# Kernel tuning notes

Hardware: AMD Instinct MI355X
Metric: run time of the kernel (lower is better)

Reference implementation:

```python
import jax, jax.numpy as jnp
import numpy as np

DIM = 4096
N_HEADS = 32
N_KV_HEADS = 8
HEAD_DIM = DIM // N_HEADS  # 128
N_REP = N_HEADS // N_KV_HEADS  # 4
BSZ_LIST = (16, 16)
START_POS_LIST = (2048, 1024)
SEQLEN = 1
CACHE_LEN = 2080
ROPE_THETA = 500000.0


def setup_inputs() -> dict:
    key = jax.random.key(0)
    ks = jax.random.split(key, 10)
    total_bsz = sum(BSZ_LIST)
    x = jax.random.normal(ks[0], (total_bsz, SEQLEN, DIM), dtype=jnp.float32)
    scale = 0.02
    wq = jax.random.normal(ks[1], (DIM, DIM), dtype=jnp.float32) * scale
    wk = jax.random.normal(ks[2], (N_KV_HEADS * HEAD_DIM, DIM), dtype=jnp.float32) * scale
    wv = jax.random.normal(ks[3], (N_KV_HEADS * HEAD_DIM, DIM), dtype=jnp.float32) * scale
    wo = jax.random.normal(ks[4], (DIM, DIM), dtype=jnp.float32) * scale
    cache_k0 = jax.random.normal(ks[5], (BSZ_LIST[0], CACHE_LEN, N_KV_HEADS, HEAD_DIM), dtype=jnp.float32)
    cache_v0 = jax.random.normal(ks[6], (BSZ_LIST[0], CACHE_LEN, N_KV_HEADS, HEAD_DIM), dtype=jnp.float32)
    cache_k1 = jax.random.normal(ks[7], (BSZ_LIST[1], CACHE_LEN, N_KV_HEADS, HEAD_DIM), dtype=jnp.float32)
    cache_v1 = jax.random.normal(ks[8], (BSZ_LIST[1], CACHE_LEN, N_KV_HEADS, HEAD_DIM), dtype=jnp.float32)
    # real RoPE tables (cos/sin of the complex freqs_cis)
    inv_freq = 1.0 / (ROPE_THETA ** (np.arange(0, HEAD_DIM, 2, dtype=np.float32) / HEAD_DIM))
    t = np.arange(CACHE_LEN, dtype=np.float32)
    ang = np.outer(t, inv_freq)  # [CACHE_LEN, HEAD_DIM/2]
    freqs_cos = jnp.asarray(np.cos(ang), dtype=jnp.float32)
    freqs_sin = jnp.asarray(np.sin(ang), dtype=jnp.float32)
    return {"x": x, "wq": wq, "wk": wk, "wv": wv, "wo": wo,
            "cache_k0": cache_k0, "cache_v0": cache_v0,
            "cache_k1": cache_k1, "cache_v1": cache_v1,
            "freqs_cos": freqs_cos, "freqs_sin": freqs_sin}


def _rope(v, cos, sin):
    # v: [b, s, h, d]; cos/sin: [s, d/2] -> interleaved complex rotation
    vr = v.reshape(v.shape[:-1] + (HEAD_DIM // 2, 2))
    a, b = vr[..., 0], vr[..., 1]
    c = cos[None, :, None, :]
    s = sin[None, :, None, :]
    out = jnp.stack([a * c - b * s, a * s + b * c], axis=-1)
    return out.reshape(v.shape)


def _group_attention(xq, xk, xv, cache_k, cache_v, start_pos, freqs_cos, freqs_sin):
    bsz, seqlen = xq.shape[0], xq.shape[1]
    cos = freqs_cos[start_pos:start_pos + seqlen]
    sin = freqs_sin[start_pos:start_pos + seqlen]
    xq = _rope(xq, cos, sin)
    xk = _rope(xk, cos, sin)
    # functional equivalent of cache[:, start_pos:start_pos+seqlen] = new; read [:start_pos+seqlen]
    keys = jnp.concatenate([cache_k[:, :start_pos], xk], axis=1)    # [b, kv, kvh, d]
    values = jnp.concatenate([cache_v[:, :start_pos], xv], axis=1)
    keys = jnp.repeat(keys, N_REP, axis=2)      # GQA repeat -> [b, kv, h, d]
    values = jnp.repeat(values, N_REP, axis=2)
    scores = jnp.einsum('bqhd,bkhd->bhqk', xq, keys) / jnp.sqrt(jnp.float32(HEAD_DIM))
    if seqlen > 1:
        kv_len = start_pos + seqlen
        q_pos = jnp.arange(seqlen)[:, None] + start_pos
        k_pos = jnp.arange(kv_len)[None, :]
        scores = jnp.where(k_pos <= q_pos, scores, jnp.float32(-jnp.inf))
    probs = jax.nn.softmax(scores.astype(jnp.float32), axis=-1).astype(xq.dtype)
    out = jnp.einsum('bhqk,bkhd->bqhd', probs, values)
    return out.reshape(bsz, seqlen, -1)


def reference(x, wq, wk, wv, wo, cache_k0, cache_v0, cache_k1, cache_v1, freqs_cos, freqs_sin):
    total_bsz, seqlen, _ = x.shape
    xq_ = x @ wq.T
    xk_ = x @ wk.T
    xv_ = x @ wv.T
    caches = ((cache_k0, cache_v0), (cache_k1, cache_v1))
    outputs = []
    start = 0
    for i, bsz in enumerate(BSZ_LIST):
        xq = xq_[start:start + bsz].reshape(bsz, seqlen, N_HEADS, HEAD_DIM)
        xk = xk_[start:start + bsz].reshape(bsz, seqlen, N_KV_HEADS, HEAD_DIM)
        xv = xv_[start:start + bsz].reshape(bsz, seqlen, N_KV_HEADS, HEAD_DIM)
        start += bsz
        ck, cv = caches[i]
        outputs.append(_group_attention(xq, xk, xv, ck, cv, START_POS_LIST[i], freqs_cos, freqs_sin))
    output = jnp.concatenate(outputs, axis=0)  # [total_bsz, seqlen, dim]
    return output @ wo.T
```

## Files before the change

kernel.cpp:

```cpp
#include <hip/hip_runtime.h>
#include <hip/hip_bf16.h>

#define DIM       4096
#define NHEADS    32
#define NKV       8
#define HD        128
#define NREP      4
#define CACHELEN  2080
#define QKVN      6144
#define BSZ       32
#define SP0       2048
#define SP1       1024
#define KCHUNK    256
#define SPLITROWS 128
#define MAXSPL    16
#define PSTRIDE   132

typedef unsigned short u16;
typedef unsigned int   u32;
typedef __bf16 bf16x8 __attribute__((ext_vector_type(8)));
typedef float  f32x4  __attribute__((ext_vector_type(4)));

#define LD8(dst, p) do { \
    *(float4*)(dst)       = *(const float4*)(p); \
    *(float4*)((dst) + 4) = *(const float4*)((p) + 4); } while (0)

static __device__ __forceinline__ bf16x8 pack8(float4 lo, float4 hi) {
    bf16x8 r;
    r[0] = (__bf16)lo.x; r[1] = (__bf16)lo.y; r[2] = (__bf16)lo.z; r[3] = (__bf16)lo.w;
    r[4] = (__bf16)hi.x; r[5] = (__bf16)hi.y; r[6] = (__bf16)hi.z; r[7] = (__bf16)hi.w;
    return r;
}

__global__ __launch_bounds__(256) void qkv_gemm(
    const float* __restrict__ x, const float* __restrict__ wq,
    const float* __restrict__ wk, const float* __restrict__ wv,
    float* __restrict__ qkv_acc)
{
    const int lane = threadIdx.x & 63;
    const int w    = threadIdx.x >> 6;
    const int n0   = (blockIdx.x * 4 + w) * 16;
    const float* W; int nr;
    if (n0 < 4096)      { W = wq; nr = n0; }
    else if (n0 < 5120) { W = wk; nr = n0 - 4096; }
    else                { W = wv; nr = n0 - 5120; }
    const int c16  = lane & 15;
    const int quad = lane >> 4;
    const int k0   = blockIdx.y * KCHUNK;
    const float* ap0 = x + (size_t)c16 * DIM + k0 + quad * 8;
    const float* ap1 = ap0 + 16 * DIM;
    const float* bp  = W + (size_t)(nr + c16) * DIM + k0 + quad * 8;
    f32x4 acc0 = {0.f,0.f,0.f,0.f}, acc1 = {0.f,0.f,0.f,0.f};
#pragma unroll 4
    for (int kk = 0; kk < KCHUNK; kk += 32) {
        bf16x8 a0 = pack8(*(const float4*)(ap0 + kk), *(const float4*)(ap0 + kk + 4));
        bf16x8 a1 = pack8(*(const float4*)(ap1 + kk), *(const float4*)(ap1 + kk + 4));
        bf16x8 b  = pack8(*(const float4*)(bp  + kk), *(const float4*)(bp  + kk + 4));
        acc0 = __builtin_amdgcn_mfma_f32_16x16x32_bf16(a0, b, acc0, 0, 0, 0);
        acc1 = __builtin_amdgcn_mfma_f32_16x16x32_bf16(a1, b, acc1, 0, 0, 0);
    }
#pragma unroll
    for (int r = 0; r < 4; ++r) {
        int m = quad * 4 + r;
        atomicAdd(&qkv_acc[(size_t)m * QKVN + n0 + c16], acc0[r]);
        atomicAdd(&qkv_acc[(size_t)(m + 16) * QKVN + n0 + c16], acc1[r]);
    }
}

__global__ __launch_bounds__(256) void attn_decode_split(
    const float* __restrict__ qkv,
    const float* __restrict__ ck0, const float* __restrict__ cv0,
    const float* __restrict__ ck1, const float* __restrict__ cv1,
    const float* __restrict__ fcos, const float* __restrict__ fsin,
    float* __restrict__ part)
{
    const int tid  = threadIdx.x;
    const int lane = tid & 63;
    const int w    = tid >> 6;
    const int quad = lane >> 4;
    const int ch   = lane & 15;
    const int db   = ch * 8;

    int b, g, s, sp;
    const float *CK, *CV;
    if ((int)blockIdx.x < 2048) {
        int bid = blockIdx.x;
        b = bid >> 7; g = (bid >> 4) & 7; s = bid & 15; sp = SP0;
        size_t off = (size_t)b * CACHELEN * NKV * HD;
        CK = ck0 + off; CV = cv0 + off;
    } else {
        int bid = blockIdx.x - 2048;
        b = 16 + (bid >> 6); g = (bid >> 3) & 7; s = bid & 7; sp = SP1;
        size_t off = (size_t)(b - 16) * CACHELEN * NKV * HD;
        CK = ck1 + off; CV = cv1 + off;
    }

    float cs[4], sn[4];
#pragma unroll
    for (int i = 0; i < 4; ++i) {
        int fi = sp * (HD / 2) + ch * 4 + i;
        cs[i] = fcos[fi];
        sn[i] = fsin[fi];
    }
    const float rs = 0.08838834764831845f;

    float qv[4][8];
#pragma unroll
    for (int h = 0; h < 4; ++h) {
        const float* qp = qkv + (size_t)b * QKVN + (g * 4 + h) * HD + db;
        float t[8];
#pragma unroll
        for (int j = 0; j < 8; ++j) t[j] = qp[j];
#pragma unroll
        for (int i = 0; i < 4; ++i) {
            float e = t[2 * i], o = t[2 * i + 1];
            qv[h][2 * i]     = (e * cs[i] - o * sn[i]) * rs;
            qv[h][2 * i + 1] = (e * sn[i] + o * cs[i]) * rs;
        }
    }

    float m_[4] = {-INFINITY, -INFINITY, -INFINITY, -INFINITY};
    float l_[4] = {0.f, 0.f, 0.f, 0.f};
    float acc[4][8];
#pragma unroll
    for (int h = 0; h < 4; ++h)
#pragma unroll
        for (int j = 0; j < 8; ++j) acc[h][j] = 0.f;

    const size_t rstride = NKV * HD;
    const float* kbase = CK + g * HD + db;
    const float* vbase = CV + g * HD + db;

    auto process2 = [&](const float* k0, const float* v0,
                        const float* k1, const float* v1) {
        float d[8];
#pragma unroll
        for (int i = 0; i < 8; ++i) d[i] = 0.f;
#pragma unroll
        for (int j = 0; j < 8; ++j) {
#pragma unroll
            for (int h = 0; h < 4; ++h) {
                d[h]     = fmaf(qv[h][j], k0[j], d[h]);
                d[4 + h] = fmaf(qv[h][j], k1[j], d[4 + h]);
            }
        }
#pragma unroll
        for (int off = 1; off < 16; off <<= 1) {
#pragma unroll
            for (int i = 0; i < 8; ++i) d[i] += __shfl_xor(d[i], off);
        }
#pragma unroll
        for (int h = 0; h < 4; ++h) {
            float mn = fmaxf(fmaxf(m_[h], d[h]), d[4 + h]);
            float sl = __expf(m_[h] - mn);
            float p0 = __expf(d[h] - mn);
            float p1 = __expf(d[4 + h] - mn);
            l_[h] = l_[h] * sl + p0 + p1;
#pragma unroll
            for (int j = 0; j < 8; ++j)
                acc[h][j] = fmaf(p1, v1[j], fmaf(p0, v0[j], acc[h][j] * sl));
            m_[h] = mn;
        }
    };

    {
        const int r0 = s * SPLITROWS + w * 8 + quad;
        const float* kp = kbase + (size_t)r0 * rstride;
        const float* vp = vbase + (size_t)r0 * rstride;
        float K0[8], V0[8], K1[8], V1[8];
        float nK0[8], nV0[8], nK1[8], nV1[8];
        LD8(K0, kp);
        LD8(K1, kp + 4 * rstride);
        LD8(V0, vp);
        LD8(V1, vp + 4 * rstride);
#pragma unroll
        for (int it = 0; it < 4; ++it) {
            if (it < 3) {
                const float* kq = kp + (size_t)(it + 1) * 32 * rstride;
                const float* vq = vp + (size_t)(it + 1) * 32 * rstride;
                LD8(nK0, kq);
                LD8(nK1, kq + 4 * rstride);
                LD8(nV0, vq);
                LD8(nV1, vq + 4 * rstride);
            }
            process2(K0, V0, K1, V1);
            if (it < 3) {
#pragma unroll
                for (int j = 0; j < 8; ++j) {
                    K0[j] = nK0[j]; K1[j] = nK1[j];
                    V0[j] = nV0[j]; V1[j] = nV1[j];
                }
            }
        }
    }

    if (s == 0) {
        float kn[8], vn[8];
        const float* kp = qkv + (size_t)b * QKVN + 4096 + g * HD + db;
        const float* vp = qkv + (size_t)b * QKVN + 5120 + g * HD + db;
        float t[8];
#pragma unroll
        for (int j = 0; j < 8; ++j) t[j] = kp[j];
#pragma unroll
        for (int i = 0; i < 4; ++i) {
            float e = t[2 * i], o = t[2 * i + 1];
            kn[2 * i]     = e * cs[i] - o * sn[i];
            kn[2 * i + 1] = e * sn[i] + o * cs[i];
        }
#pragma unroll
        for (int j = 0; j < 8; ++j) vn[j] = vp[j];

        float d0 = 0.f, d1 = 0.f, d2 = 0.f, d3 = 0.f;
#pragma unroll
        for (int j = 0; j < 8; ++j) {
            d0 = fmaf(qv[0][j], kn[j], d0);
            d1 = fmaf(qv[1][j], kn[j], d1);
            d2 = fmaf(qv[2][j], kn[j], d2);
            d3 = fmaf(qv[3][j], kn[j], d3);
        }
#pragma unroll
        for (int off = 1; off < 16; off <<= 1) {
            d0 += __shfl_xor(d0, off);
            d1 += __shfl_xor(d1, off);
            d2 += __shfl_xor(d2, off);
            d3 += __shfl_xor(d3, off);
        }
        if (w == 0 && quad == 0) {
            float sc[4] = {d0, d1, d2, d3};
#pragma unroll
            for (int h = 0; h < 4; ++h) {
                float mn = fmaxf(m_[h], sc[h]);
                float sl = __expf(m_[h] - mn);
                float p  = __expf(sc[h] - mn);
                l_[h] = l_[h] * sl + p;
#pragma unroll
                for (int j = 0; j < 8; ++j)
                    acc[h][j] = fmaf(acc[h][j], sl, p * vn[j]);
                m_[h] = mn;
            }
        }
    }

#pragma unroll
    for (int off = 16; off <= 32; off <<= 1) {
#pragma unroll
        for (int h = 0; h < 4; ++h) {
            float mo = __shfl_xor(m_[h], off);
            float lo = __shfl_xor(l_[h], off);
            float ao[8];
#pragma unroll
            for (int j = 0; j < 8; ++j) ao[j] = __shfl_xor(acc[h][j], off);
            float mn = fmaxf(m_[h], mo);
            float s1 = __expf(m_[h] - mn);
            float s2 = __expf(mo - mn);
            l_[h] = l_[h] * s1 + lo * s2;
#pragma unroll
            for (int j = 0; j < 8; ++j) acc[h][j] = acc[h][j] * s1 + ao[j] * s2;
            m_[h] = mn;
        }
    }

    __shared__ float ls_m[4][4][16];
    __shared__ float ls_l[4][4][16];
    __shared__ float ls_a[4][4][16][8];
    if (quad == 0) {
#pragma unroll
        for (int h = 0; h < 4; ++h) {
            ls_m[w][h][ch] = m_[h];
            ls_l[w][h][ch] = l_[h];
#pragma unroll
            for (int j = 0; j < 8; ++j) ls_a[w][h][ch][j] = acc[h][j];
        }
    }
    __syncthreads();
    if (tid < 64) {
        int h = tid >> 4, c = tid & 15;
        float mm = -INFINITY, ll = 0.f, ac[8] = {0.f,0.f,0.f,0.f,0.f,0.f,0.f,0.f};
#pragma unroll
        for (int w2 = 0; w2 < 4; ++w2) {
            float m2 = ls_m[w2][h][c], l2 = ls_l[w2][h][c];
            float mn = fmaxf(mm, m2);
            float s1 = __expf(mm - mn), s2 = __expf(m2 - mn);
            ll = ll * s1 + l2 * s2;
#pragma unroll
            for (int j = 0; j < 8; ++j) ac[j] = ac[j] * s1 + ls_a[w2][h][c][j] * s2;
            mm = mn;
        }
        int bg = b * 8 + g;
        float* pp = part + ((((size_t)bg * MAXSPL + s) * 4 + h) * PSTRIDE);
        float4 o0, o1;
        o0.x = ac[0]; o0.y = ac[1]; o0.z = ac[2]; o0.w = ac[3];
        o1.x = ac[4]; o1.y = ac[5]; o1.z = ac[6]; o1.w = ac[7];
        *(float4*)(pp + c * 8)     = o0;
        *(float4*)(pp + c * 8 + 4) = o1;
        if (c == 0) { pp[128] = mm; pp[129] = ll; }
    }
}

__global__ __launch_bounds__(64) void attn_reduce(
    const float* __restrict__ part, float* __restrict__ attn)
{
    const int lane = threadIdx.x;
    const int h = lane >> 4, c = lane & 15;
    const int bg = blockIdx.x;
    const int b = bg >> 3, g = bg & 7;
    const int nspl = (b < 16) ? (SP0 / SPLITROWS) : (SP1 / SPLITROWS);
    const float* pb = part + (size_t)bg * MAXSPL * 4 * PSTRIDE;

    float mm = -INFINITY, ll = 0.f, ac[8] = {0.f,0.f,0.f,0.f,0.f,0.f,0.f,0.f};
    for (int s = 0; s < nspl; ++s) {
        const float* pp = pb + ((size_t)s * 4 + h) * PSTRIDE;
        float m2 = pp[128], l2 = pp[129];
        float4 a0 = *(const float4*)(pp + c * 8);
        float4 a1 = *(const float4*)(pp + c * 8 + 4);
        float a2[8] = {a0.x, a0.y, a0.z, a0.w, a1.x, a1.y, a1.z, a1.w};
        float mn = fmaxf(mm, m2);
        float s1 = __expf(mm - mn), s2 = __expf(m2 - mn);
        ll = ll * s1 + l2 * s2;
#pragma unroll
        for (int j = 0; j < 8; ++j) ac[j] = ac[j] * s1 + a2[j] * s2;
        mm = mn;
    }
    float inv = 1.f / ll;
    float* op = attn + (size_t)b * DIM + (g * 4 + h) * HD + c * 8;
    float4 o0, o1;
    o0.x = ac[0] * inv; o0.y = ac[1] * inv; o0.z = ac[2] * inv; o0.w = ac[3] * inv;
    o1.x = ac[4] * inv; o1.y = ac[5] * inv; o1.z = ac[6] * inv; o1.w = ac[7] * inv;
    *(float4*)op       = o0;
    *(float4*)(op + 4) = o1;
}

__global__ __launch_bounds__(256) void out_gemm(
    const float* __restrict__ A, const float* __restrict__ wo,
    float* __restrict__ out)
{
    const int lane = threadIdx.x & 63;
    const int w    = threadIdx.x >> 6;
    const int n0   = (blockIdx.x * 4 + w) * 16;
    const int c16  = lane & 15;
    const int quad = lane >> 4;
    const int k0   = blockIdx.y * KCHUNK;
    const float* ap0 = A + (size_t)c16 * DIM + k0 + quad * 8;
    const float* ap1 = ap0 + 16 * DIM;
    const float* bp  = wo + (size_t)(n0 + c16) * DIM + k0 + quad * 8;
    f32x4 acc0 = {0.f,0.f,0.f,0.f}, acc1 = {0.f,0.f,0.f,0.f};
#pragma unroll 4
    for (int kk = 0; kk < KCHUNK; kk += 32) {
        bf16x8 a0 = pack8(*(const float4*)(ap0 + kk), *(const float4*)(ap0 + kk + 4));
        bf16x8 a1 = pack8(*(const float4*)(ap1 + kk), *(const float4*)(ap1 + kk + 4));
        bf16x8 b  = pack8(*(const float4*)(bp  + kk), *(const float4*)(bp  + kk + 4));
        acc0 = __builtin_amdgcn_mfma_f32_16x16x32_bf16(a0, b, acc0, 0, 0, 0);
        acc1 = __builtin_amdgcn_mfma_f32_16x16x32_bf16(a1, b, acc1, 0, 0, 0);
    }
#pragma unroll
    for (int r = 0; r < 4; ++r) {
        int m = quad * 4 + r;
        atomicAdd(&out[(size_t)m * DIM + n0 + c16], acc0[r]);
        atomicAdd(&out[(size_t)(m + 16) * DIM + n0 + c16], acc1[r]);
    }
}

extern "C" void kernel_launch(void* const* d_in, const int* in_sizes, int n_in,
                              void* d_out, int out_size, void* d_ws, size_t ws_size,
                              hipStream_t stream)
{
    const float* x   = (const float*)d_in[0];
    const float* wq  = (const float*)d_in[1];
    const float* wk  = (const float*)d_in[2];
    const float* wv  = (const float*)d_in[3];
    const float* wo  = (const float*)d_in[4];
    const float* ck0 = (const float*)d_in[5];
    const float* cv0 = (const float*)d_in[6];
    const float* ck1 = (const float*)d_in[7];
    const float* cv1 = (const float*)d_in[8];
    const float* fc  = (const float*)d_in[9];
    const float* fs  = (const float*)d_in[10];

    float* qkv_acc = (float*)d_ws;
    float* attn    = qkv_acc + BSZ * QKVN;
    float* part    = attn + BSZ * DIM;
    float* out     = (float*)d_out;

    hipMemsetAsync(qkv_acc, 0, (size_t)(BSZ * QKVN) * sizeof(float), stream);
    hipMemsetAsync(out, 0, (size_t)(BSZ * DIM) * sizeof(float), stream);

    qkv_gemm<<<dim3(QKVN / 64, DIM / KCHUNK), 256, 0, stream>>>(x, wq, wk, wv, qkv_acc);
    attn_decode_split<<<dim3(2048 + 1024), 256, 0, stream>>>(qkv_acc, ck0, cv0, ck1, cv1, fc, fs, part);
    attn_reduce<<<dim3(BSZ * NKV), 64, 0, stream>>>(part, attn);
    out_gemm<<<dim3(DIM / 64, DIM / KCHUNK), 256, 0, stream>>>(attn, wo, out);
}
```

Before: 589.7 us.

## Replace atomic split-K with partial buffers and batch attention loads per split

```diff
diff --git a/kernel.cpp b/kernel.cpp
--- a/kernel.cpp
+++ b/kernel.cpp
@@ -11,9 +11,10 @@
 #define BSZ       32
 #define SP0       2048
 #define SP1       1024
-#define KCHUNK    256
-#define SPLITROWS 128
-#define MAXSPL    16
+#define KCHUNK    512
+#define NSPLK     8
+#define SPLITROWS 256
+#define MAXSPL    8
 #define PSTRIDE   132
 
 typedef unsigned short u16;
@@ -35,7 +36,7 @@
 __global__ __launch_bounds__(256) void qkv_gemm(
     const float* __restrict__ x, const float* __restrict__ wq,
     const float* __restrict__ wk, const float* __restrict__ wv,
-    float* __restrict__ qkv_acc)
+    float* __restrict__ qkv_part)
 {
     const int lane = threadIdx.x & 63;
     const int w    = threadIdx.x >> 6;
@@ -59,12 +60,27 @@
         acc0 = __builtin_amdgcn_mfma_f32_16x16x32_bf16(a0, b, acc0, 0, 0, 0);
         acc1 = __builtin_amdgcn_mfma_f32_16x16x32_bf16(a1, b, acc1, 0, 0, 0);
     }
+    float* dst = qkv_part + (size_t)blockIdx.y * (BSZ * QKVN);
 #pragma unroll
     for (int r = 0; r < 4; ++r) {
         int m = quad * 4 + r;
-        atomicAdd(&qkv_acc[(size_t)m * QKVN + n0 + c16], acc0[r]);
-        atomicAdd(&qkv_acc[(size_t)(m + 16) * QKVN + n0 + c16], acc1[r]);
-    }
+        dst[(size_t)m * QKVN + n0 + c16]        = acc0[r];
+        dst[(size_t)(m + 16) * QKVN + n0 + c16] = acc1[r];
+    }
+}
+
+__global__ __launch_bounds__(256) void sum_splits(
+    const float4* __restrict__ in, float4* __restrict__ out, int n4)
+{
+    int i = blockIdx.x * 256 + threadIdx.x;
+    if (i >= n4) return;
+    float4 s0 = in[i];
+#pragma unroll
+    for (int s = 1; s < NSPLK; ++s) {
+        float4 t = in[(size_t)s * n4 + i];
+        s0.x += t.x; s0.y += t.y; s0.z += t.z; s0.w += t.w;
+    }
+    out[i] = s0;
 }
 
 __global__ __launch_bounds__(256) void attn_decode_split(
@@ -83,14 +99,14 @@
 
     int b, g, s, sp;
     const float *CK, *CV;
-    if ((int)blockIdx.x < 2048) {
+    if ((int)blockIdx.x < 1024) {
         int bid = blockIdx.x;
-        b = bid >> 7; g = (bid >> 4) & 7; s = bid & 15; sp = SP0;
+        b = bid >> 6; g = (bid >> 3) & 7; s = bid & 7; sp = SP0;
         size_t off = (size_t)b * CACHELEN * NKV * HD;
         CK = ck0 + off; CV = cv0 + off;
     } else {
-        int bid = blockIdx.x - 2048;
-        b = 16 + (bid >> 6); g = (bid >> 3) & 7; s = bid & 7; sp = SP1;
+        int bid = blockIdx.x - 1024;
+        b = 16 + (bid >> 5); g = (bid >> 2) & 7; s = bid & 3; sp = SP1;
         size_t off = (size_t)(b - 16) * CACHELEN * NKV * HD;
         CK = ck1 + off; CV = cv1 + off;
     }
@@ -119,83 +135,9 @@
         }
     }
 
-    float m_[4] = {-INFINITY, -INFINITY, -INFINITY, -INFINITY};
-    float l_[4] = {0.f, 0.f, 0.f, 0.f};
-    float acc[4][8];
-#pragma unroll
-    for (int h = 0; h < 4; ++h)
-#pragma unroll
-        for (int j = 0; j < 8; ++j) acc[h][j] = 0.f;
-
-    const size_t rstride = NKV * HD;
-    const float* kbase = CK + g * HD + db;
-    const float* vbase = CV + g * HD + db;
-
-    auto process2 = [&](const float* k0, const float* v0,
-                        const float* k1, const float* v1) {
-        float d[8];
-#pragma unroll
-        for (int i = 0; i < 8; ++i) d[i] = 0.f;
-#pragma unroll
-        for (int j = 0; j < 8; ++j) {
-#pragma unroll
-            for (int h = 0; h < 4; ++h) {
-                d[h]     = fmaf(qv[h][j], k0[j], d[h]);
-                d[4 + h] = fmaf(qv[h][j], k1[j], d[4 + h]);
-            }
-        }
-#pragma unroll
-        for (int off = 1; off < 16; off <<= 1) {
-#pragma unroll
-            for (int i = 0; i < 8; ++i) d[i] += __shfl_xor(d[i], off);
-        }
-#pragma unroll
-        for (int h = 0; h < 4; ++h) {
-            float mn = fmaxf(fmaxf(m_[h], d[h]), d[4 + h]);
-            float sl = __expf(m_[h] - mn);
-            float p0 = __expf(d[h] - mn);
-            float p1 = __expf(d[4 + h] - mn);
-            l_[h] = l_[h] * sl + p0 + p1;
-#pragma unroll
-            for (int j = 0; j < 8; ++j)
-                acc[h][j] = fmaf(p1, v1[j], fmaf(p0, v0[j], acc[h][j] * sl));
-            m_[h] = mn;
-        }
-    };
-
-    {
-        const int r0 = s * SPLITROWS + w * 8 + quad;
-        const float* kp = kbase + (size_t)r0 * rstride;
-        const float* vp = vbase + (size_t)r0 * rstride;
-        float K0[8], V0[8], K1[8], V1[8];
-        float nK0[8], nV0[8], nK1[8], nV1[8];
-        LD8(K0, kp);
-        LD8(K1, kp + 4 * rstride);
-        LD8(V0, vp);
-        LD8(V1, vp + 4 * rstride);
-#pragma unroll
-        for (int it = 0; it < 4; ++it) {
-            if (it < 3) {
-                const float* kq = kp + (size_t)(it + 1) * 32 * rstride;
-                const float* vq = vp + (size_t)(it + 1) * 32 * rstride;
-                LD8(nK0, kq);
-                LD8(nK1, kq + 4 * rstride);
-                LD8(nV0, vq);
-                LD8(nV1, vq + 4 * rstride);
-            }
-            process2(K0, V0, K1, V1);
-            if (it < 3) {
-#pragma unroll
-                for (int j = 0; j < 8; ++j) {
-                    K0[j] = nK0[j]; K1[j] = nK1[j];
-                    V0[j] = nV0[j]; V1[j] = nV1[j];
-                }
-            }
-        }
-    }
-
-    if (s == 0) {
-        float kn[8], vn[8];
+    const bool has_new = (s == 0) && (w == 0);
+    float kn[8], vn[8];
+    if (has_new) {
         const float* kp = qkv + (size_t)b * QKVN + 4096 + g * HD + db;
         const float* vp = qkv + (size_t)b * QKVN + 5120 + g * HD + db;
         float t[8];
@@ -209,68 +151,144 @@
         }
 #pragma unroll
         for (int j = 0; j < 8; ++j) vn[j] = vp[j];
-
-        float d0 = 0.f, d1 = 0.f, d2 = 0.f, d3 = 0.f;
-#pragma unroll
-        for (int j = 0; j < 8; ++j) {
-            d0 = fmaf(qv[0][j], kn[j], d0);
-            d1 = fmaf(qv[1][j], kn[j], d1);
-            d2 = fmaf(qv[2][j], kn[j], d2);
-            d3 = fmaf(qv[3][j], kn[j], d3);
-        }
-#pragma unroll
-        for (int off = 1; off < 16; off <<= 1) {
-            d0 += __shfl_xor(d0, off);
-            d1 += __shfl_xor(d1, off);
-            d2 += __shfl_xor(d2, off);
-            d3 += __shfl_xor(d3, off);
-        }
-        if (w == 0 && quad == 0) {
-            float sc[4] = {d0, d1, d2, d3};
-#pragma unroll
-            for (int h = 0; h < 4; ++h) {
-                float mn = fmaxf(m_[h], sc[h]);
-                float sl = __expf(m_[h] - mn);
-                float p  = __expf(sc[h] - mn);
-                l_[h] = l_[h] * sl + p;
-#pragma unroll
-                for (int j = 0; j < 8; ++j)
-                    acc[h][j] = fmaf(acc[h][j], sl, p * vn[j]);
-                m_[h] = mn;
+    }
+
+    float m_[4] = {-INFINITY, -INFINITY, -INFINITY, -INFINITY};
+    float l_[4] = {0.f, 0.f, 0.f, 0.f};
+    float acc[4][8];
+#pragma unroll
+    for (int h = 0; h < 4; ++h)
+#pragma unroll
+        for (int j = 0; j < 8; ++j) acc[h][j] = 0.f;
+
+    const size_t rstride = NKV * HD;
+    const float* kp0 = CK + g * HD + db + (size_t)(s * SPLITROWS + w * 8 + quad) * rstride;
+    const float* vp0 = CV + g * HD + db + (size_t)(s * SPLITROWS + w * 8 + quad) * rstride;
+
+    auto do_batch = [&](const float* kpB, const float* vpB, bool fold_new) {
+        float Ka[4][2][8];
+#pragma unroll
+        for (int it = 0; it < 4; ++it) {
+            const float* kq = kpB + (size_t)(it * 32) * rstride;
+            LD8(Ka[it][0], kq);
+            LD8(Ka[it][1], kq + 4 * rstride);
+        }
+        float d[4][2][4];
+#pragma unroll
+        for (int it = 0; it < 4; ++it)
+#pragma unroll
+            for (int r = 0; r < 2; ++r)
+#pragma unroll
+                for (int h = 0; h < 4; ++h) d[it][r][h] = 0.f;
+#pragma unroll
+        for (int it = 0; it < 4; ++it)
+#pragma unroll
+            for (int j = 0; j < 8; ++j)
+#pragma unroll
+                for (int h = 0; h < 4; ++h) {
+                    d[it][0][h] = fmaf(qv[h][j], Ka[it][0][j], d[it][0][h]);
+                    d[it][1][h] = fmaf(qv[h][j], Ka[it][1][j], d[it][1][h]);
+                }
+#pragma unroll
+        for (int off = 1; off < 16; off <<= 1)
+#pragma unroll
+            for (int it = 0; it < 4; ++it)
+#pragma unroll
+                for (int r = 0; r < 2; ++r)
+#pragma unroll
+                    for (int h = 0; h < 4; ++h)
+                        d[it][r][h] += __shfl_xor(d[it][r][h], off);
+        float bm[4];
+#pragma unroll
+        for (int h = 0; h < 4; ++h) {
+            float a0 = fmaxf(fmaxf(d[0][0][h], d[0][1][h]), fmaxf(d[1][0][h], d[1][1][h]));
+            float a1 = fmaxf(fmaxf(d[2][0][h], d[2][1][h]), fmaxf(d[3][0][h], d[3][1][h]));
+            bm[h] = fmaxf(a0, a1);
+        }
+#pragma unroll
+        for (int off = 16; off <= 32; off <<= 1)
+#pragma unroll
+            for (int h = 0; h < 4; ++h)
+                bm[h] = fmaxf(bm[h], __shfl_xor(bm[h], off));
+        float dn[4] = {0.f, 0.f, 0.f, 0.f};
+        if (fold_new) {
+#pragma unroll
+            for (int j = 0; j < 8; ++j)
+#pragma unroll
+                for (int h = 0; h < 4; ++h) dn[h] = fmaf(qv[h][j], kn[j], dn[h]);
+#pragma unroll
+            for (int off = 1; off < 16; off <<= 1)
+#pragma unroll
+                for (int h = 0; h < 4; ++h) dn[h] += __shfl_xor(dn[h], off);
+#pragma unroll
+            for (int h = 0; h < 4; ++h) bm[h] = fmaxf(bm[h], dn[h]);
+        }
+        float Va[4][2][8];
+#pragma unroll
+        for (int it = 0; it < 4; ++it) {
+            const float* vq = vpB + (size_t)(it * 32) * rstride;
+            LD8(Va[it][0], vq);
+            LD8(Va[it][1], vq + 4 * rstride);
+        }
+#pragma unroll
+        for (int h = 0; h < 4; ++h) {
+            float mn = fmaxf(m_[h], bm[h]);
+            float sl = __expf(m_[h] - mn);
+            float lb = 0.f;
+#pragma unroll
+            for (int it = 0; it < 4; ++it)
+#pragma unroll
+                for (int r = 0; r < 2; ++r) {
+                    float p = __expf(d[it][r][h] - mn);
+                    d[it][r][h] = p;
+                    lb += p;
+                }
+            l_[h] = l_[h] * sl + lb;
+#pragma unroll
+            for (int j = 0; j < 8; ++j) {
+                float a = acc[h][j] * sl;
+#pragma unroll
+                for (int it = 0; it < 4; ++it) {
+                    a = fmaf(d[it][0][h], Va[it][0][j], a);
+                    a = fmaf(d[it][1][h], Va[it][1][j], a);
+                }
+                acc[h][j] = a;
             }
-        }
-    }
+            m_[h] = mn;
+            if (fold_new && quad == 0) {
+                float pn = __expf(dn[h] - mn);
+                l_[h] += pn;
+#pragma unroll
+                for (int j = 0; j < 8; ++j) acc[h][j] = fmaf(pn, vn[j], acc[h][j]);
+            }
+        }
+    };
+
+    do_batch(kp0, vp0, false);
+    do_batch(kp0 + 128 * rstride, vp0 + 128 * rstride, has_new);
 
 #pragma unroll
     for (int off = 16; off <= 32; off <<= 1) {
 #pragma unroll
         for (int h = 0; h < 4; ++h) {
-            float mo = __shfl_xor(m_[h], off);
-            float lo = __shfl_xor(l_[h], off);
-            float ao[8];
-#pragma unroll
-            for (int j = 0; j < 8; ++j) ao[j] = __shfl_xor(acc[h][j], off);
-            float mn = fmaxf(m_[h], mo);
-            float s1 = __expf(m_[h] - mn);
-            float s2 = __expf(mo - mn);
-            l_[h] = l_[h] * s1 + lo * s2;
-#pragma unroll
-            for (int j = 0; j < 8; ++j) acc[h][j] = acc[h][j] * s1 + ao[j] * s2;
-            m_[h] = mn;
-        }
-    }
-
-    __shared__ float ls_m[4][4][16];
-    __shared__ float ls_l[4][4][16];
+            l_[h] += __shfl_xor(l_[h], off);
+#pragma unroll
+            for (int j = 0; j < 8; ++j) acc[h][j] += __shfl_xor(acc[h][j], off);
+        }
+    }
+
+    __shared__ float ls_m[4][4];
+    __shared__ float ls_l[4][4];
     __shared__ float ls_a[4][4][16][8];
+    if (lane == 0) {
+#pragma unroll
+        for (int h = 0; h < 4; ++h) { ls_m[w][h] = m_[h]; ls_l[w][h] = l_[h]; }
+    }
     if (quad == 0) {
 #pragma unroll
-        for (int h = 0; h < 4; ++h) {
-            ls_m[w][h][ch] = m_[h];
-            ls_l[w][h][ch] = l_[h];
+        for (int h = 0; h < 4; ++h)
 #pragma unroll
             for (int j = 0; j < 8; ++j) ls_a[w][h][ch][j] = acc[h][j];
-        }
     }
     __syncthreads();
     if (tid < 64) {
@@ -278,7 +296,7 @@
         float mm = -INFINITY, ll = 0.f, ac[8] = {0.f,0.f,0.f,0.f,0.f,0.f,0.f,0.f};
 #pragma unroll
         for (int w2 = 0; w2 < 4; ++w2) {
-            float m2 = ls_m[w2][h][c], l2 = ls_l[w2][h][c];
+            float m2 = ls_m[w2][h], l2 = ls_l[w2][h];
             float mn = fmaxf(mm, m2);
             float s1 = __expf(mm - mn), s2 = __expf(m2 - mn);
             ll = ll * s1 + l2 * s2;
@@ -332,7 +350,7 @@
 
 __global__ __launch_bounds__(256) void out_gemm(
     const float* __restrict__ A, const float* __restrict__ wo,
-    float* __restrict__ out)
+    float* __restrict__ out_part)
 {
     const int lane = threadIdx.x & 63;
     const int w    = threadIdx.x >> 6;
@@ -352,11 +370,12 @@
         acc0 = __builtin_amdgcn_mfma_f32_16x16x32_bf16(a0, b, acc0, 0, 0, 0);
         acc1 = __builtin_amdgcn_mfma_f32_16x16x32_bf16(a1, b, acc1, 0, 0, 0);
     }
+    float* dst = out_part + (size_t)blockIdx.y * (BSZ * DIM);
 #pragma unroll
     for (int r = 0; r < 4; ++r) {
         int m = quad * 4 + r;
-        atomicAdd(&out[(size_t)m * DIM + n0 + c16], acc0[r]);
-        atomicAdd(&out[(size_t)(m + 16) * DIM + n0 + c16], acc1[r]);
+        dst[(size_t)m * DIM + n0 + c16]        = acc0[r];
+        dst[(size_t)(m + 16) * DIM + n0 + c16] = acc1[r];
     }
 }
 
@@ -376,16 +395,17 @@
     const float* fc  = (const float*)d_in[9];
     const float* fs  = (const float*)d_in[10];
 
-    float* qkv_acc = (float*)d_ws;
-    float* attn    = qkv_acc + BSZ * QKVN;
-    float* part    = attn + BSZ * DIM;
+    float* W = (float*)d_ws;
+    float* gparts  = W;
+    float* qkv     = gparts + (size_t)NSPLK * BSZ * QKVN;
+    float* part    = qkv + BSZ * QKVN;
+    float* attn    = part + (size_t)BSZ * NKV * MAXSPL * 4 * PSTRIDE;
     float* out     = (float*)d_out;
 
-    hipMemsetAsync(qkv_acc, 0, (size_t)(BSZ * QKVN) * sizeof(float), stream);
-    hipMemsetAsync(out, 0, (size_t)(BSZ * DIM) * sizeof(float), stream);
-
-    qkv_gemm<<<dim3(QKVN / 64, DIM / KCHUNK), 256, 0, stream>>>(x, wq, wk, wv, qkv_acc);
-    attn_decode_split<<<dim3(2048 + 1024), 256, 0, stream>>>(qkv_acc, ck0, cv0, ck1, cv1, fc, fs, part);
+    qkv_gemm<<<dim3(QKVN / 64, NSPLK), 256, 0, stream>>>(x, wq, wk, wv, gparts);
+    sum_splits<<<dim3(BSZ * QKVN / 1024), 256, 0, stream>>>((const float4*)gparts, (float4*)qkv, BSZ * QKVN / 4);
+    attn_decode_split<<<dim3(1024 + 512), 256, 0, stream>>>(qkv, ck0, cv0, ck1, cv1, fc, fs, part);
     attn_reduce<<<dim3(BSZ * NKV), 64, 0, stream>>>(part, attn);
-    out_gemm<<<dim3(DIM / 64, DIM / KCHUNK), 256, 0, stream>>>(attn, wo, out);
-}
+    out_gemm<<<dim3(DIM / 64, NSPLK), 256, 0, stream>>>(attn, wo, gparts);
+    sum_splits<<<dim3(BSZ * DIM / 1024), 256, 0, stream>>>((const float4*)gparts, (float4*)out, BSZ * DIM / 4);
+}
```

Result: faster. 571.7 us (-3.0%).
